# Performance work log

Hardware: AMD Instinct MI355X
Metric: run time of the kernel (lower is better)

Reference implementation:

```python
import jax, jax.numpy as jnp
import numpy as np

N_NODES = 100000
N_EDGES = 1600000
D_FEAT = 32
D_HID = 64
D_OUT = 64


def setup_inputs() -> dict:
    key = jax.random.key(0)
    ks = jax.random.split(key, 7)
    x = jax.random.normal(ks[0], (N_NODES, D_FEAT), dtype=jnp.float32)
    pos = jax.random.uniform(ks[1], (N_NODES, 3), dtype=jnp.float32) * 100.0
    # Fixed-size stand-in for radius_graph(pos, 5) output: (2, E) [source; target]
    edge_index = jax.random.randint(ks[2], (2, N_EDGES), 0, N_NODES, dtype=jnp.int64)
    d_in = D_FEAT + 3  # concat(x_j, pos_j - pos_i)
    W1 = jax.random.normal(ks[3], (d_in, D_HID), dtype=jnp.float32) / np.sqrt(d_in)
    b1 = jnp.zeros((D_HID,), dtype=jnp.float32)
    W2 = jax.random.normal(ks[4], (D_HID, D_OUT), dtype=jnp.float32) / np.sqrt(D_HID)
    b2 = jnp.zeros((D_OUT,), dtype=jnp.float32)
    return {"x": x, "pos": pos, "edge_index": edge_index,
            "W1": W1, "b1": b1, "W2": W2, "b2": b2}


def reference(x, pos, edge_index, W1, b1, W2, b2):
    n = x.shape[0]
    # PointNetConv default add_self_loops=True (radius_graph used loop=False)
    loops = jnp.arange(n, dtype=edge_index.dtype)
    src = jnp.concatenate([edge_index[0], loops])  # source j
    dst = jnp.concatenate([edge_index[1], loops])  # target i
    # gather: per-edge message input [E+N, d_feat+3]
    msg_in = jnp.concatenate([x[src], pos[src] - pos[dst]], axis=-1)
    # local_nn MLP
    h = jax.nn.relu(msg_in @ W1 + b1) @ W2 + b2
    # scatter: max-aggregate onto target nodes (PointConv aggr='max')
    out = jax.ops.segment_max(h, dst, num_segments=n)
    return out
```

## Files before the change

kernel.cpp:

```cpp
#include <hip/hip_runtime.h>
#include <hip/hip_bf16.h>
#include <math.h>

#define N_NODES 100000
#define N_EDGES 1600000
#define D_FEAT 32
#define D_HID 64
#define D_OUT 64
#define CAP 48
#define NPB 64
#define NBKT 1563
#define ECAP 1536
#define B1 200
#define E_PER_B1 8000
#define NB_NODE 1024

typedef short bf16x8 __attribute__((ext_vector_type(8)));
typedef float f32x4  __attribute__((ext_vector_type(4)));

__device__ inline unsigned short f2bf(float f) {
    unsigned u = __float_as_uint(f);
    u += 0x7fff + ((u >> 16) & 1);
    return (unsigned short)(u >> 16);
}
__device__ inline float bf2f(unsigned short h) {
    return __uint_as_float(((unsigned)h) << 16);
}
__device__ inline unsigned pack2bf(float lo, float hi) {
    return ((unsigned)f2bf(hi) << 16) | (unsigned)f2bf(lo);
}

union afu { uint4 u; bf16x8 v; };

__device__ inline afu abuild(uint4 vv, const float* qk) {
    afu af;
#pragma unroll
    for (int m = 0; m < 4; ++m) {
        unsigned w = (&vv.x)[m];
        float flo = __uint_as_float(w << 16);
        float fhi = __uint_as_float(w & 0xFFFF0000u);
        float hlo = fmaxf(flo - qk[2 * m],     0.0f);
        float hhi = fmaxf(fhi - qk[2 * m + 1], 0.0f);
        (&af.u.x)[m] = pack2bf(hlo, hhi);
    }
    return af;
}

__global__ __launch_bounds__(256)
void node_kernel(const float* __restrict__ x,
                 const float* __restrict__ pos,
                 const float* __restrict__ W1,
                 const float* __restrict__ b1,
                 unsigned short* __restrict__ vb,
                 unsigned short* __restrict__ qb) {
    const int lane = threadIdx.x & 63;
    const int wid  = (blockIdx.x * blockDim.x + threadIdx.x) >> 6;
    const int nw   = (NB_NODE * 256) >> 6;

    float w[D_FEAT + 3];
#pragma unroll
    for (int f = 0; f < D_FEAT + 3; ++f)
        w[f] = W1[f * D_HID + lane];
    const float bb = b1[lane];

    for (int node = wid; node < N_NODES; node += nw) {
        const float* xr = x + (size_t)node * D_FEAT;
        float acc = bb;
#pragma unroll
        for (int f = 0; f < D_FEAT; ++f)
            acc = fmaf(xr[f], w[f], acc);

        const float* pr = pos + (size_t)node * 3;
        float qa = 0.0f;
#pragma unroll
        for (int p = 0; p < 3; ++p)
            qa = fmaf(pr[p], w[D_FEAT + p], qa);

        vb[(size_t)node * D_HID + lane] = f2bf(acc + qa);
        qb[(size_t)node * D_HID + lane] = f2bf(qa);
    }
}

__global__ __launch_bounds__(1024)
void bin_kernel(const int* __restrict__ src,
                const int* __restrict__ dst,
                int* __restrict__ gcnt,
                unsigned int* __restrict__ coarse) {
    __shared__ int hist[NBKT];
    const int tid = threadIdx.x;
    const int e0 = blockIdx.x * E_PER_B1;
    const int nq = E_PER_B1 / 4;

    for (int b = tid; b < NBKT; b += 1024) hist[b] = 0;
    __syncthreads();

    const int4* d4p = (const int4*)(dst + e0);
    const int4* s4p = (const int4*)(src + e0);

    for (int i = tid; i < nq; i += 1024) {
        int4 d4 = d4p[i];
        atomicAdd(&hist[d4.x >> 6], 1);
        atomicAdd(&hist[d4.y >> 6], 1);
        atomicAdd(&hist[d4.z >> 6], 1);
        atomicAdd(&hist[d4.w >> 6], 1);
    }
    __syncthreads();

    for (int b = tid; b < NBKT; b += 1024) {
        int c = hist[b];
        hist[b] = (c > 0) ? atomicAdd(&gcnt[b], c) : 0;
    }
    __syncthreads();

    for (int i = tid; i < nq; i += 1024) {
        int4 d4 = d4p[i];
        int4 s4 = s4p[i];
        int p0 = atomicAdd(&hist[d4.x >> 6], 1);
        int p1 = atomicAdd(&hist[d4.y >> 6], 1);
        int p2 = atomicAdd(&hist[d4.z >> 6], 1);
        int p3 = atomicAdd(&hist[d4.w >> 6], 1);
        if (p0 < ECAP) coarse[(size_t)(d4.x >> 6) * ECAP + p0] = ((unsigned)s4.x << 6) | (unsigned)(d4.x & 63);
        if (p1 < ECAP) coarse[(size_t)(d4.y >> 6) * ECAP + p1] = ((unsigned)s4.y << 6) | (unsigned)(d4.y & 63);
        if (p2 < ECAP) coarse[(size_t)(d4.z >> 6) * ECAP + p2] = ((unsigned)s4.z << 6) | (unsigned)(d4.z & 63);
        if (p3 < ECAP) coarse[(size_t)(d4.w >> 6) * ECAP + p3] = ((unsigned)s4.w << 6) | (unsigned)(d4.w & 63);
    }
}

__global__ __launch_bounds__(256)
void agg_kernel(const unsigned short* __restrict__ vb,
                const unsigned short* __restrict__ qb,
                const float* __restrict__ W2,
                const float* __restrict__ b2,
                const int* __restrict__ gcnt,
                const unsigned int* __restrict__ coarse,
                float* __restrict__ out) {
    __shared__ int lcnt[NPB];
    __shared__ int lslots[NPB][CAP];

    const int tid  = threadIdx.x;
    const int lane = tid & 63;
    const int wave = tid >> 6;
    const int quad = lane >> 4;
    const int mrow = lane & 15;
    const int bkt  = blockIdx.x;
    const int nbase = bkt << 6;

    bf16x8 bfrag[4][2];
#pragma unroll
    for (int t = 0; t < 4; ++t)
#pragma unroll
        for (int kh = 0; kh < 2; ++kh) {
            bf16x8 f;
#pragma unroll
            for (int j = 0; j < 8; ++j)
                f[j] = (short)f2bf(W2[(kh * 32 + quad * 8 + j) * D_OUT + t * 16 + mrow]);
            bfrag[t][kh] = f;
        }
    float bias[4];
#pragma unroll
    for (int t = 0; t < 4; ++t) bias[t] = b2[t * 16 + mrow];

    int E_b = gcnt[bkt];
    if (E_b > ECAP) E_b = ECAP;
    for (int i = tid; i < NPB; i += 256) lcnt[i] = 0;
    __syncthreads();
    for (int i = tid; i < E_b; i += 256) {
        unsigned enc = coarse[(size_t)bkt * ECAP + i];
        int local = (int)(enc & 63u);
        int s     = (int)(enc >> 6);
        int p = atomicAdd(&lcnt[local], 1);
        if (p < CAP) lslots[local][p] = s;
    }
    __syncthreads();

    for (int ln = wave; ln < NPB; ln += 4) {
        const int node = nbase + ln;
        if (node >= N_NODES) break;

        float qf[2][8];
#pragma unroll
        for (int kh = 0; kh < 2; ++kh) {
            bf16x8 qv = *(const bf16x8*)(qb + (size_t)node * D_HID + kh * 32 + quad * 8);
#pragma unroll
            for (int j = 0; j < 8; ++j) qf[kh][j] = bf2f((unsigned short)qv[j]);
        }

        int deg = lcnt[ln];
        if (deg > CAP) deg = CAP;
        const int rows = deg + 1;
        const int npair = (rows + 31) >> 5;

        float rmax[4][4];
#pragma unroll
        for (int t = 0; t < 4; ++t)
#pragma unroll
            for (int r = 0; r < 4; ++r) rmax[t][r] = -INFINITY;

        const uint4* vbq = (const uint4*)vb;
        for (int p = 0; p < npair; ++p) {
            int ia = (p << 5) + mrow;
            int ib = ia + 16;
            int sA = (ia < deg) ? lslots[ln][ia] : node;
            int sB = (ib < deg) ? lslots[ln][ib] : node;

            const uint4* pa = vbq + (size_t)sA * 8 + quad;
            const uint4* pb = vbq + (size_t)sB * 8 + quad;
            uint4 vA0 = pa[0], vA1 = pa[4];
            uint4 vB0 = pb[0], vB1 = pb[4];

            afu aA0 = abuild(vA0, qf[0]);
            afu aA1 = abuild(vA1, qf[1]);
            afu aB0 = abuild(vB0, qf[0]);
            afu aB1 = abuild(vB1, qf[1]);

#pragma unroll
            for (int t = 0; t < 4; ++t) {
                f32x4 accA = (f32x4){0.f, 0.f, 0.f, 0.f};
                f32x4 accB = (f32x4){0.f, 0.f, 0.f, 0.f};
                accA = __builtin_amdgcn_mfma_f32_16x16x32_bf16(aA0.v, bfrag[t][0], accA, 0, 0, 0);
                accB = __builtin_amdgcn_mfma_f32_16x16x32_bf16(aB0.v, bfrag[t][0], accB, 0, 0, 0);
                accA = __builtin_amdgcn_mfma_f32_16x16x32_bf16(aA1.v, bfrag[t][1], accA, 0, 0, 0);
                accB = __builtin_amdgcn_mfma_f32_16x16x32_bf16(aB1.v, bfrag[t][1], accB, 0, 0, 0);
#pragma unroll
                for (int r = 0; r < 4; ++r)
                    rmax[t][r] = fmaxf(rmax[t][r], fmaxf(accA[r], accB[r]));
            }
        }

        float fin[4];
#pragma unroll
        for (int t = 0; t < 4; ++t) {
            float m = fmaxf(fmaxf(rmax[t][0], rmax[t][1]), fmaxf(rmax[t][2], rmax[t][3]));
            m = fmaxf(m, __shfl_xor(m, 16, 64));
            m = fmaxf(m, __shfl_xor(m, 32, 64));
            fin[t] = m + bias[t];
        }
        float r = (quad == 0) ? fin[0] : (quad == 1) ? fin[1] : (quad == 2) ? fin[2] : fin[3];
        out[(size_t)node * D_OUT + lane] = r;
    }
}

extern "C" void kernel_launch(void* const* d_in, const int* in_sizes, int n_in,
                              void* d_out, int out_size, void* d_ws, size_t ws_size,
                              hipStream_t stream) {
    const float* x   = (const float*)d_in[0];
    const float* pos = (const float*)d_in[1];
    const int*   ei  = (const int*)d_in[2];
    const float* W1  = (const float*)d_in[3];
    const float* b1  = (const float*)d_in[4];
    const float* W2  = (const float*)d_in[5];
    const float* b2  = (const float*)d_in[6];
    float* out = (float*)d_out;

    char* ws = (char*)d_ws;
    unsigned short* vb   = (unsigned short*)ws;
    unsigned short* qb   = (unsigned short*)(ws + 12800000);
    int*            gcnt = (int*)(ws + 25600000);
    unsigned int* coarse = (unsigned int*)(ws + 25610240);

    const int* src = ei;
    const int* dst = ei + N_EDGES;

    (void)hipMemsetAsync(gcnt, 0, NBKT * sizeof(int), stream);
    hipLaunchKernelGGL(bin_kernel, dim3(B1), dim3(1024), 0, stream,
                       src, dst, gcnt, coarse);
    hipLaunchKernelGGL(node_kernel, dim3(NB_NODE), dim3(256), 0, stream,
                       x, pos, W1, b1, vb, qb);
    hipLaunchKernelGGL(agg_kernel, dim3(NBKT), dim3(256), 0, stream,
                       vb, qb, W2, b2, gcnt, coarse, out);
}
```

Before: 223.9 us.

## Coarsen edge binning to 256-node buckets and batch edges in sixteens

The binning kernel now groups edges into 391 buckets of 256 destination nodes instead of 1563 buckets of 64, so its shared histogram is smaller and there are fewer global bucket atomics. Each aggregation block still handles 64 nodes, but it scans the whole 256-node bucket row and keeps only the edges for its quarter, so the coarse edge list is read four times. The per-node MFMA loop now processes 16 edge rows per step instead of 32, with the next source index prefetched from shared memory, which reduces padded rows for low-degree nodes.

Measured after the change: 232.9 us. 1.04x slower.

```diff
diff --git a/kernel.cpp b/kernel.cpp
--- a/kernel.cpp
+++ b/kernel.cpp
@@ -9,8 +9,10 @@
 #define D_OUT 64
 #define CAP 48
 #define NPB 64
-#define NBKT 1563
-#define ECAP 1536
+#define NSB 1563
+#define BKT_NODES 256
+#define NBKT 391
+#define ECAP 4608
 #define B1 200
 #define E_PER_B1 8000
 #define NB_NODE 1024
@@ -99,10 +101,10 @@
 
     for (int i = tid; i < nq; i += 1024) {
         int4 d4 = d4p[i];
-        atomicAdd(&hist[d4.x >> 6], 1);
-        atomicAdd(&hist[d4.y >> 6], 1);
-        atomicAdd(&hist[d4.z >> 6], 1);
-        atomicAdd(&hist[d4.w >> 6], 1);
+        atomicAdd(&hist[d4.x >> 8], 1);
+        atomicAdd(&hist[d4.y >> 8], 1);
+        atomicAdd(&hist[d4.z >> 8], 1);
+        atomicAdd(&hist[d4.w >> 8], 1);
     }
     __syncthreads();
 
@@ -115,14 +117,14 @@
     for (int i = tid; i < nq; i += 1024) {
         int4 d4 = d4p[i];
         int4 s4 = s4p[i];
-        int p0 = atomicAdd(&hist[d4.x >> 6], 1);
-        int p1 = atomicAdd(&hist[d4.y >> 6], 1);
-        int p2 = atomicAdd(&hist[d4.z >> 6], 1);
-        int p3 = atomicAdd(&hist[d4.w >> 6], 1);
-        if (p0 < ECAP) coarse[(size_t)(d4.x >> 6) * ECAP + p0] = ((unsigned)s4.x << 6) | (unsigned)(d4.x & 63);
-        if (p1 < ECAP) coarse[(size_t)(d4.y >> 6) * ECAP + p1] = ((unsigned)s4.y << 6) | (unsigned)(d4.y & 63);
-        if (p2 < ECAP) coarse[(size_t)(d4.z >> 6) * ECAP + p2] = ((unsigned)s4.z << 6) | (unsigned)(d4.z & 63);
-        if (p3 < ECAP) coarse[(size_t)(d4.w >> 6) * ECAP + p3] = ((unsigned)s4.w << 6) | (unsigned)(d4.w & 63);
+        int p0 = atomicAdd(&hist[d4.x >> 8], 1);
+        int p1 = atomicAdd(&hist[d4.y >> 8], 1);
+        int p2 = atomicAdd(&hist[d4.z >> 8], 1);
+        int p3 = atomicAdd(&hist[d4.w >> 8], 1);
+        if (p0 < ECAP) coarse[(size_t)(d4.x >> 8) * ECAP + p0] = ((unsigned)s4.x << 8) | (unsigned)(d4.x & 255);
+        if (p1 < ECAP) coarse[(size_t)(d4.y >> 8) * ECAP + p1] = ((unsigned)s4.y << 8) | (unsigned)(d4.y & 255);
+        if (p2 < ECAP) coarse[(size_t)(d4.z >> 8) * ECAP + p2] = ((unsigned)s4.z << 8) | (unsigned)(d4.z & 255);
+        if (p3 < ECAP) coarse[(size_t)(d4.w >> 8) * ECAP + p3] = ((unsigned)s4.w << 8) | (unsigned)(d4.w & 255);
     }
 }
 
@@ -142,8 +144,10 @@
     const int wave = tid >> 6;
     const int quad = lane >> 4;
     const int mrow = lane & 15;
-    const int bkt  = blockIdx.x;
-    const int nbase = bkt << 6;
+    const int sb   = blockIdx.x;
+    const int bkt  = sb >> 2;
+    const int qsel = sb & 3;
+    const int nbase = sb << 6;
 
     bf16x8 bfrag[4][2];
 #pragma unroll
@@ -164,12 +168,15 @@
     if (E_b > ECAP) E_b = ECAP;
     for (int i = tid; i < NPB; i += 256) lcnt[i] = 0;
     __syncthreads();
+    const unsigned int* crow = coarse + (size_t)bkt * ECAP;
     for (int i = tid; i < E_b; i += 256) {
-        unsigned enc = coarse[(size_t)bkt * ECAP + i];
-        int local = (int)(enc & 63u);
-        int s     = (int)(enc >> 6);
-        int p = atomicAdd(&lcnt[local], 1);
-        if (p < CAP) lslots[local][p] = s;
+        unsigned enc = crow[i];
+        int local = (int)(enc & 255u);
+        if ((local >> 6) == qsel) {
+            int ln = local & 63;
+            int p = atomicAdd(&lcnt[ln], 1);
+            if (p < CAP) lslots[ln][p] = (int)(enc >> 8);
+        }
     }
     __syncthreads();
 
@@ -188,7 +195,8 @@
         int deg = lcnt[ln];
         if (deg > CAP) deg = CAP;
         const int rows = deg + 1;
-        const int npair = (rows + 31) >> 5;
+        const int nbat = (rows + 15) >> 4;
+        const int* lsl = lslots[ln];
 
         float rmax[4][4];
 #pragma unroll
@@ -197,34 +205,27 @@
             for (int r = 0; r < 4; ++r) rmax[t][r] = -INFINITY;
 
         const uint4* vbq = (const uint4*)vb;
-        for (int p = 0; p < npair; ++p) {
-            int ia = (p << 5) + mrow;
-            int ib = ia + 16;
-            int sA = (ia < deg) ? lslots[ln][ia] : node;
-            int sB = (ib < deg) ? lslots[ln][ib] : node;
-
-            const uint4* pa = vbq + (size_t)sA * 8 + quad;
-            const uint4* pb = vbq + (size_t)sB * 8 + quad;
-            uint4 vA0 = pa[0], vA1 = pa[4];
-            uint4 vB0 = pb[0], vB1 = pb[4];
-
-            afu aA0 = abuild(vA0, qf[0]);
-            afu aA1 = abuild(vA1, qf[1]);
-            afu aB0 = abuild(vB0, qf[0]);
-            afu aB1 = abuild(vB1, qf[1]);
+        int s_cur = (mrow < deg) ? lsl[mrow] : node;
+        for (int b = 0; b < nbat; ++b) {
+            int idx = (b + 1) * 16 + mrow;
+            int s_nxt = (idx < deg) ? lsl[idx] : node;
+
+            const uint4* pa = vbq + (size_t)s_cur * 8 + quad;
+            uint4 v0 = pa[0], v1 = pa[4];
+
+            afu a0 = abuild(v0, qf[0]);
+            afu a1 = abuild(v1, qf[1]);
 
 #pragma unroll
             for (int t = 0; t < 4; ++t) {
-                f32x4 accA = (f32x4){0.f, 0.f, 0.f, 0.f};
-                f32x4 accB = (f32x4){0.f, 0.f, 0.f, 0.f};
-                accA = __builtin_amdgcn_mfma_f32_16x16x32_bf16(aA0.v, bfrag[t][0], accA, 0, 0, 0);
-                accB = __builtin_amdgcn_mfma_f32_16x16x32_bf16(aB0.v, bfrag[t][0], accB, 0, 0, 0);
-                accA = __builtin_amdgcn_mfma_f32_16x16x32_bf16(aA1.v, bfrag[t][1], accA, 0, 0, 0);
-                accB = __builtin_amdgcn_mfma_f32_16x16x32_bf16(aB1.v, bfrag[t][1], accB, 0, 0, 0);
+                f32x4 acc = (f32x4){0.f, 0.f, 0.f, 0.f};
+                acc = __builtin_amdgcn_mfma_f32_16x16x32_bf16(a0.v, bfrag[t][0], acc, 0, 0, 0);
+                acc = __builtin_amdgcn_mfma_f32_16x16x32_bf16(a1.v, bfrag[t][1], acc, 0, 0, 0);
 #pragma unroll
                 for (int r = 0; r < 4; ++r)
-                    rmax[t][r] = fmaxf(rmax[t][r], fmaxf(accA[r], accB[r]));
+                    rmax[t][r] = fmaxf(rmax[t][r], acc[r]);
             }
+            s_cur = s_nxt;
         }
 
         float fin[4];
@@ -266,6 +267,6 @@
                        src, dst, gcnt, coarse);
     hipLaunchKernelGGL(node_kernel, dim3(NB_NODE), dim3(256), 0, stream,
                        x, pos, W1, b1, vb, qb);
-    hipLaunchKernelGGL(agg_kernel, dim3(NBKT), dim3(256), 0, stream,
+    hipLaunchKernelGGL(agg_kernel, dim3(NSB), dim3(256), 0, stream,
                        vb, qb, W2, b2, gcnt, coarse, out);
 }
```
